# Optimization experiments

Hardware: AMD Instinct MI355X
Metric: run time of the kernel (lower is better)

Reference implementation:

```python
import jax, jax.numpy as jnp
import numpy as np

D_MODEL, HEADS, GROUPS, DIM_HEAD = 256, 8, 8, 64
INNER = HEADS * DIM_HEAD              # 512
OFF_DIMS = INNER // GROUPS            # 64 channels fed to the offset network per group
DF, OFF_SCALE, KS, PAD = 4, 4.0, 6, 1  # downsample_factor, offset_scale, kernel, (6-4)//2
CPB_DIM = D_MODEL // 4                # 64
NUM_LAYERS = 6
SCALE = DIM_HEAD ** -0.5
B, H, W = 1, 40, 40


def grouped_conv1x1(x, w, g):
    # x: (b, cin, h, w); w: (cout, cin//g) torch grouped 1x1 conv weight (squeezed)
    b, cin, h, wd = x.shape
    cout = w.shape[0]
    xg = x.reshape(b, g, cin // g, h, wd)
    wg = w.reshape(g, cout // g, cin // g)
    return jnp.einsum('goi,bgihw->bgohw', wg, xg).reshape(b, cout, h, wd)


def create_grid(h, w, dtype):
    # torch meshgrid(arange(w), arange(h), indexing='xy') stacked at dim 0
    ys, xs = jnp.meshgrid(jnp.arange(h, dtype=dtype), jnp.arange(w, dtype=dtype), indexing='ij')
    return jnp.stack((xs, ys))  # (2, h, w): channel0 = x, channel1 = y


def normalize_grid(grid):
    # faithful to source: channel0 scaled by (h-1), channel1 by (w-1); out dim last
    h, w = grid.shape[-2:]
    g0 = 2.0 * grid[..., 0, :, :] / max(h - 1, 1) - 1.0
    g1 = 2.0 * grid[..., 1, :, :] / max(w - 1, 1) - 1.0
    return jnp.stack((g0, g1), axis=-1)


def grid_sample_bilinear(img, grid):
    # torch F.grid_sample, mode='bilinear', padding_mode='zeros', align_corners=False
    Bn, C, Hh, Ww = img.shape
    gx = ((grid[..., 0] + 1.0) * Ww - 1.0) * 0.5
    gy = ((grid[..., 1] + 1.0) * Hh - 1.0) * 0.5
    x0 = jnp.floor(gx)
    y0 = jnp.floor(gy)
    wx1 = gx - x0
    wy1 = gy - y0
    flat = img.reshape(Bn, C, Hh * Ww)

    def gather(xi, yi):
        valid = (xi >= 0) & (xi <= Ww - 1) & (yi >= 0) & (yi <= Hh - 1)
        xc = jnp.clip(xi, 0, Ww - 1).astype(jnp.int32)
        yc = jnp.clip(yi, 0, Hh - 1).astype(jnp.int32)
        idx = (yc * Ww + xc).reshape(Bn, 1, -1)
        vals = jnp.take_along_axis(flat, idx, axis=2).reshape(Bn, C, *xi.shape[1:])
        return vals * valid[:, None].astype(img.dtype)

    return (gather(x0, y0) * ((1 - wx1) * (1 - wy1))[:, None]
            + gather(x0 + 1, y0) * (wx1 * (1 - wy1))[:, None]
            + gather(x0, y0 + 1) * ((1 - wx1) * wy1)[:, None]
            + gather(x0 + 1, y0 + 1) * (wx1 * wy1)[:, None])


def deform_attn(x, wq, wk, wv, w_off1, b_off1, w_off2,
                cpb_w0, cpb_b0, cpb_w1, cpb_b1, cpb_w2, cpb_b2, w_out, b_out):
    b, c, Hh, Ww = x.shape
    bg = b * GROUPS
    q = grouped_conv1x1(x, wq, GROUPS)                      # (b, 512, H, W)
    qg = q.reshape(bg, OFF_DIMS, Hh, Ww)                    # group heads: (b g) d h w
    # offset network: depthwise 6x6 stride-4 conv -> GELU -> 1x1 -> tanh * scale
    off = jax.lax.conv_general_dilated(
        qg, w_off1, (DF, DF), ((PAD, PAD), (PAD, PAD)),
        dimension_numbers=('NCHW', 'OIHW', 'NCHW'), feature_group_count=OFF_DIMS)
    off = jax.nn.gelu(off + b_off1[None, :, None, None], approximate=False)
    off = jnp.tanh(jnp.einsum('oc,bchw->bohw', w_off2, off)) * OFF_SCALE  # (bg,2,h',w')
    hp, wp = off.shape[-2:]
    vgrid = create_grid(hp, wp, x.dtype)[None] + off
    vgrid_scaled = normalize_grid(vgrid)                    # (bg, h', w', 2)
    xg = x.reshape(bg, c // GROUPS, Hh, Ww)
    kv = grid_sample_bilinear(xg, vgrid_scaled).reshape(b, c, hp, wp)
    k = grouped_conv1x1(kv, wk, GROUPS)
    v = grouped_conv1x1(kv, wv, GROUPS)
    i, j = Hh * Ww, hp * wp
    qh = (q * SCALE).reshape(b, HEADS, DIM_HEAD, i).transpose(0, 1, 3, 2)  # bhid
    kh = k.reshape(b, HEADS, DIM_HEAD, j).transpose(0, 1, 3, 2)
    vh = v.reshape(b, HEADS, DIM_HEAD, j).transpose(0, 1, 3, 2)
    sim = jnp.einsum('bhid,bhjd->bhij', qh, kh)
    # continuous positional bias (CPB, depth-2 MLP on signed-log relative coords)
    grid_q = normalize_grid(create_grid(Hh, Ww, x.dtype)).reshape(i, 2)
    grid_kv = vgrid_scaled.reshape(bg, j, 2)
    pos = grid_q[None, :, None, :] - grid_kv[:, None, :, :]  # (bg, i, j, 2)
    bias = jnp.sign(pos) * jnp.log1p(jnp.abs(pos))
    bias = jax.nn.relu(bias @ cpb_w0.T + cpb_b0)
    bias = jax.nn.relu(bias @ cpb_w1.T + cpb_b1)
    bias = bias @ cpb_w2.T + cpb_b2                          # (bg, i, j, 1)
    sim = sim + bias.reshape(b, GROUPS, i, j)                # heads//offset_groups == 1
    attn = jax.nn.softmax(sim, axis=-1)                      # stable softmax (matches amax-subtract)
    out = jnp.einsum('bhij,bhjd->bhid', attn, vh)
    out = out.transpose(0, 1, 3, 2).reshape(b, INNER, Hh, Ww)
    return jnp.einsum('oc,bchw->bohw', w_out, out) + b_out[None, :, None, None]


def setup_inputs() -> dict:
    key = jax.random.key(0)
    ks = jax.random.split(key, 16)
    L = NUM_LAYERS

    def p(k, shape, scale=0.02):
        return jax.random.normal(k, shape, dtype=jnp.float32) * scale

    return {
        'bev_feat': jax.random.normal(ks[0], (B, D_MODEL, H, W), dtype=jnp.float32),
        'wq': p(ks[1], (L, INNER, D_MODEL // GROUPS)),
        'wk': p(ks[2], (L, INNER, D_MODEL // GROUPS)),
        'wv': p(ks[3], (L, INNER, D_MODEL // GROUPS)),
        'w_off1': p(ks[4], (L, OFF_DIMS, 1, KS, KS)),
        'b_off1': jnp.zeros((L, OFF_DIMS), jnp.float32),
        'w_off2': p(ks[5], (L, 2, OFF_DIMS)),
        'cpb_w0': p(ks[6], (L, CPB_DIM, 2), 0.5),
        'cpb_b0': jnp.zeros((L, CPB_DIM), jnp.float32),
        'cpb_w1': p(ks[7], (L, CPB_DIM, CPB_DIM), 0.1),
        'cpb_b1': jnp.zeros((L, CPB_DIM), jnp.float32),
        'cpb_w2': p(ks[8], (L, 1, CPB_DIM), 0.1),
        'cpb_b2': jnp.zeros((L, 1), jnp.float32),
        'w_out': p(ks[9], (L, D_MODEL, INNER)),
        'b_out': jnp.zeros((L, D_MODEL), jnp.float32),
    }


def reference(bev_feat, wq, wk, wv, w_off1, b_off1, w_off2,
              cpb_w0, cpb_b0, cpb_w1, cpb_b1, cpb_w2, cpb_b2, w_out, b_out):
    # The source encoder loop runs `output = layer(bev_feat)` on the ORIGINAL
    # input each iteration, so only the last layer's output survives. Faithful
    # math = apply layer NUM_LAYERS-1 once (dropout in eval mode -> identity).
    l = NUM_LAYERS - 1
    return deform_attn(bev_feat, wq[l], wk[l], wv[l], w_off1[l], b_off1[l], w_off2[l],
                       cpb_w0[l], cpb_b0[l], cpb_w1[l], cpb_b1[l], cpb_w2[l], cpb_b2[l],
                       w_out[l], b_out[l])
```

## Files before the change

kernel.cpp:

```cpp
#include <hip/hip_runtime.h>
#include <math.h>


#define NP 1600
#define NJ 100

typedef _Float16 f16x8 __attribute__((ext_vector_type(8)));
typedef _Float16 f16x4 __attribute__((ext_vector_type(4)));
typedef _Float16 f16x2 __attribute__((ext_vector_type(2)));
typedef float  f32x4  __attribute__((ext_vector_type(4)));
typedef float  f32x2  __attribute__((ext_vector_type(2)));

template<int CTRL>
__device__ __forceinline__ float dpp_add(float x) {
  int y = __builtin_amdgcn_update_dpp(0, __builtin_bit_cast(int, x),
                                      CTRL, 0xf, 0xf, true);
  return x + __builtin_bit_cast(float, y);
}

__global__ __launch_bounds__(256, 4) void k_off_cpb(
    const float* __restrict__ x, const float* __restrict__ wq,
    const float* __restrict__ wdw,
    const float* __restrict__ bdw, const float* __restrict__ wo2,
    const float* __restrict__ wk, const float* __restrict__ wv,
    const float* __restrict__ w0, const float* __restrict__ b0,
    const float* __restrict__ w1, const float* __restrict__ b1v,
    const float* __restrict__ cw2, const float* __restrict__ b2,
    float* __restrict__ kout, float* __restrict__ vout_t,
    _Float16* __restrict__ bias16) {
  __shared__ float x_lds[36][32];
  __shared__ float psum[4][72];
  __shared__ float su_l[40];
  __shared__ float sv_l[40];
  __shared__ _Float16 a16[40][72];
  __shared__ _Float16 c16[40][72];
  int b = blockIdx.x;
  int g = b & 7;
  int j = b >> 3;
  int gj = g * 100 + j;
  int t = threadIdx.x;
  int lane = t & 63;
  int wv_id = t >> 6;
  int oy = j / 10, ox = j - (j / 10) * 10;
  int row = lane & 15;
  int kgrp = lane >> 4;

  for (int idx = t; idx < 1152; idx += 256) {
    int tap = idx >> 5, ci = idx & 31;
    int ky = tap / 6, kx = tap - (tap / 6) * 6;
    int iy = oy * 4 - 1 + ky;
    int ix = ox * 4 - 1 + kx;
    float v = 0.f;
    if (iy >= 0 && iy < 40 && ix >= 0 && ix < 40)
      v = x[(g * 32 + ci) * NP + iy * 40 + ix];
    x_lds[tap][ci] = v;
  }
  __syncthreads();

  {
    float wqreg[32];
    const float* wqr = wq + (size_t)(g * 64 + lane) * 32;
#pragma unroll
    for (int q4 = 0; q4 < 8; ++q4) {
      f32x4 a = *(const f32x4*)(wqr + q4 * 4);
#pragma unroll
      for (int e = 0; e < 4; ++e) wqreg[q4 * 4 + e] = a[e];
    }
    float acc = 0.f;
#pragma unroll
    for (int tu = 0; tu < 9; ++tu) {
      int tt = wv_id * 9 + tu;
      float qv = 0.f;
#pragma unroll
      for (int q4 = 0; q4 < 8; ++q4) {
        f32x4 xv = *(const f32x4*)&x_lds[tt][q4 * 4];
#pragma unroll
        for (int e = 0; e < 4; ++e)
          qv = fmaf(wqreg[q4 * 4 + e], xv[e], qv);
      }
      acc = fmaf(wdw[lane * 36 + tt], qv, acc);
    }
    psum[wv_id][lane] = acc;
  }
  __syncthreads();

  if (wv_id == 0) {
    float accd = psum[0][lane] + psum[1][lane] + psum[2][lane] + psum[3][lane]
               + bdw[lane];
    float od = 0.5f * accd * (1.0f + erff(accd * 0.70710678118654752440f));
    float px = wo2[lane] * od, py = wo2[64 + lane] * od;
#pragma unroll
    for (int m = 1; m < 64; m <<= 1) {
      px += __shfl_xor(px, m);
      py += __shfl_xor(py, m);
    }
    float ax = tanhf(px) * 4.f;
    float ay = tanhf(py) * 4.f;
    float vx = (float)ox + ax;
    float vy = (float)oy + ay;
    float g0 = 2.f * vx / 9.f - 1.f;
    float g1 = 2.f * vy / 9.f - 1.f;
    if (lane < 40) {
      float qc = (float)lane * (2.f / 39.f) - 1.f;
      float u = qc - g0;
      float vv2 = qc - g1;
      su_l[lane] = copysignf(log1pf(fabsf(u)), u);
      sv_l[lane] = copysignf(log1pf(fabsf(vv2)), vv2);
    }
    float gx = ((g0 + 1.f) * 40.f - 1.f) * 0.5f;
    float gy = ((g1 + 1.f) * 40.f - 1.f) * 0.5f;
    float x0f = floorf(gx), y0f = floorf(gy);
    float wx = gx - x0f, wy = gy - y0f;
    bool mx0 = (x0f >= 0.f) && (x0f <= 39.f);
    bool mx1 = (x0f + 1.f >= 0.f) && (x0f + 1.f <= 39.f);
    bool my0 = (y0f >= 0.f) && (y0f <= 39.f);
    bool my1 = (y0f + 1.f >= 0.f) && (y0f + 1.f <= 39.f);
    int ix0 = (int)fminf(fmaxf(x0f, 0.f), 39.f);
    int ix1 = (int)fminf(fmaxf(x0f + 1.f, 0.f), 39.f);
    int iy0 = (int)fminf(fmaxf(y0f, 0.f), 39.f);
    int iy1 = (int)fminf(fmaxf(y0f + 1.f, 0.f), 39.f);
    float w00 = (1.f - wx) * (1.f - wy) * ((mx0 && my0) ? 1.f : 0.f);
    float w10 = wx * (1.f - wy) * ((mx1 && my0) ? 1.f : 0.f);
    float w01 = (1.f - wx) * wy * ((mx0 && my1) ? 1.f : 0.f);
    float w11 = wx * wy * ((mx1 && my1) ? 1.f : 0.f);
    int b00 = iy0 * 40 + ix0, b10 = iy0 * 40 + ix1;
    int b01 = iy1 * 40 + ix0, b11 = iy1 * 40 + ix1;
    float kvc = 0.f;
    if (lane < 32) {
      const float* xc = x + (g * 32 + lane) * NP;
      kvc = w00 * xc[b00] + w10 * xc[b10] + w01 * xc[b01] + w11 * xc[b11];
    }
    const float* wkr = wk + (g * 64 + lane) * 32;
    const float* wvr = wv + (g * 64 + lane) * 32;
    float wkreg[32], wvreg[32];
#pragma unroll
    for (int q4 = 0; q4 < 8; ++q4) {
      f32x4 a = *(const f32x4*)(wkr + q4 * 4);
      f32x4 bq = *(const f32x4*)(wvr + q4 * 4);
#pragma unroll
      for (int e = 0; e < 4; ++e) { wkreg[q4 * 4 + e] = a[e]; wvreg[q4 * 4 + e] = bq[e]; }
    }
    float kacc = 0.f, vacc = 0.f;
#pragma unroll
    for (int c = 0; c < 32; ++c) {
      float kvb = __shfl(kvc, c);
      kacc = fmaf(wkreg[c], kvb, kacc);
      vacc = fmaf(wvreg[c], kvb, vacc);
    }
    kout[(g * 64 + lane) * 100 + j] = kacc;
    vout_t[(size_t)gj * 64 + lane] = vacc;
  }
  __syncthreads();

  for (int idx = t; idx < 2560; idx += 256) {
    int xi = idx >> 6, kk = idx & 63;
    a16[xi][kk] = (_Float16)fmaf(w0[2 * kk], su_l[xi], b0[kk]);
    c16[xi][kk] = (_Float16)(w0[2 * kk + 1] * sv_l[xi]);
  }

  f16x8 B[4][2];
#pragma unroll
  for (int ct = 0; ct < 4; ++ct)
#pragma unroll
    for (int s = 0; s < 2; ++s)
#pragma unroll
      for (int e = 0; e < 8; ++e)
        B[ct][s][e] = (_Float16)w1[(ct * 16 + row) * 64 + s * 32 + kgrp * 8 + e];
  float b1c[4], w2c[4];
#pragma unroll
  for (int ct = 0; ct < 4; ++ct) {
    b1c[ct] = b1v[ct * 16 + row];
    w2c[ct] = cw2[ct * 16 + row];
  }
  float bb = b2[0];
  _Float16* outp = bias16 + (size_t)gj * 1600;
  __syncthreads();

  int it0 = wv_id * 25;
  int iy = wv_id * 10;
  int ix = row;
  f16x8 zero8 = {};
  for (int it = it0; it < it0 + 25; ++it) {
    f32x4 acc[4];
#pragma unroll
    for (int ct = 0; ct < 4; ++ct) {
      acc[ct][0] = 0.f; acc[ct][1] = 0.f; acc[ct][2] = 0.f; acc[ct][3] = 0.f;
    }
#pragma unroll
    for (int s = 0; s < 2; ++s) {
      f16x8 av = *(const f16x8*)&a16[ix][s * 32 + kgrp * 8];
      f16x8 cv = *(const f16x8*)&c16[iy][s * 32 + kgrp * 8];
      f16x8 A = __builtin_elementwise_max(av + cv, zero8);
#pragma unroll
      for (int ct = 0; ct < 4; ++ct)
        acc[ct] = __builtin_amdgcn_mfma_f32_16x16x32_f16(A, B[ct][s], acc[ct], 0, 0, 0);
    }
    float part[4];
#pragma unroll
    for (int ri = 0; ri < 4; ++ri) {
      float s2 = 0.f;
#pragma unroll
      for (int ct = 0; ct < 4; ++ct) {
        float val = acc[ct][ri] + b1c[ct];
        s2 = fmaf(w2c[ct], fmaxf(val, 0.f), s2);
      }
      part[ri] = s2;
    }
#pragma unroll
    for (int ri = 0; ri < 4; ++ri) {
      part[ri] = dpp_add<0xB1>(part[ri]);
      part[ri] = dpp_add<0x4E>(part[ri]);
      part[ri] = dpp_add<0x141>(part[ri]);
      part[ri] = dpp_add<0x140>(part[ri]);
    }
    if (row == 0) {
      f16x4 o;
      o[0] = (_Float16)(part[0] + bb); o[1] = (_Float16)(part[1] + bb);
      o[2] = (_Float16)(part[2] + bb); o[3] = (_Float16)(part[3] + bb);
      *(f16x4*)(outp + it * 16 + kgrp * 4) = o;
    }
    ix += 16;
    if (ix >= 40) { ix -= 40; ++iy; }
  }
}

__global__ __launch_bounds__(256) void k_attn(
    const float* __restrict__ x, const float* __restrict__ wq,
    const float* __restrict__ k, const float* __restrict__ v_t,
    const _Float16* __restrict__ bias16, float* __restrict__ inner) {
  __shared__ float v_lds[100][68];
  __shared__ float s_lds[16][100];
  __shared__ float q_lds[64][20];
  __shared__ float x_tile[32][16];
  int h = blockIdx.x / 100;
  int i0 = (blockIdx.x - h * 100) * 16;
  int t = threadIdx.x;
  for (int idx = t; idx < 6400; idx += 256) {
    int j = idx >> 6, d = idx & 63;
    v_lds[j][d] = v_t[(size_t)h * 6400 + idx];
  }
  for (int idx = t; idx < 512; idx += 256) {
    int ci = idx >> 4, i = idx & 15;
    x_tile[ci][i] = x[(h * 32 + ci) * NP + i0 + i];
  }
  __syncthreads();
  {
    int d = t & 63;
    int i4 = t >> 6;
    f32x4 wr[8];
#pragma unroll
    for (int qq = 0; qq < 8; ++qq)
      wr[qq] = *(const f32x4*)(wq + (size_t)(h * 64 + d) * 32 + qq * 4);
#pragma unroll
    for (int ii = 0; ii < 4; ++ii) {
      int i = i4 * 4 + ii;
      float acc = 0.f;
#pragma unroll
      for (int ci = 0; ci < 32; ++ci)
        acc = fmaf(wr[ci >> 2][ci & 3], x_tile[ci][i], acc);
      q_lds[d][i] = acc;
    }
  }
  __syncthreads();
  if (t < 200) {
    int ib = (t / 25) * 2, jb = (t % 25) * 4;
    const float* kp = k + h * 64 * 100 + jb;
    float a[2][4];
#pragma unroll
    for (int ii = 0; ii < 2; ++ii)
#pragma unroll
      for (int jj = 0; jj < 4; ++jj) a[ii][jj] = 0.f;
#pragma unroll 8
    for (int d = 0; d < 64; ++d) {
      f32x2 qv = *(const f32x2*)&q_lds[d][ib];
      f32x4 kv4 = *(const f32x4*)(kp + d * 100);
#pragma unroll
      for (int ii = 0; ii < 2; ++ii)
#pragma unroll
        for (int jj = 0; jj < 4; ++jj)
          a[ii][jj] = fmaf(qv[ii], kv4[jj], a[ii][jj]);
    }
    const _Float16* bcol = bias16 + (size_t)h * 100 * 1600;
#pragma unroll
    for (int jj = 0; jj < 4; ++jj) {
      f16x2 bv = *(const f16x2*)(bcol + (size_t)(jb + jj) * 1600 + i0 + ib);
#pragma unroll
      for (int ii = 0; ii < 2; ++ii)
        s_lds[ib + ii][jb + jj] = fmaf(a[ii][jj], 0.125f, (float)bv[ii]);
    }
  }
  __syncthreads();
  {
    int i = t >> 4, sub = t & 15;
    float m = -1e30f;
    for (int j = sub; j < 100; j += 16) m = fmaxf(m, s_lds[i][j]);
#pragma unroll
    for (int off = 1; off < 16; off <<= 1) m = fmaxf(m, __shfl_xor(m, off));
    float sum = 0.f;
    for (int j = sub; j < 100; j += 16) {
      float e = expf(s_lds[i][j] - m);
      s_lds[i][j] = e;
      sum += e;
    }
#pragma unroll
    for (int off = 1; off < 16; off <<= 1) sum += __shfl_xor(sum, off);
    float inv = 1.f / sum;
    for (int j = sub; j < 100; j += 16) s_lds[i][j] *= inv;
  }
  __syncthreads();
  {
    int i = t & 15, db = (t >> 4) * 4;
    float acc[4];
#pragma unroll
    for (int dd = 0; dd < 4; ++dd) acc[dd] = 0.f;
    for (int jc = 0; jc < 25; ++jc) {
      f32x4 sv = *(const f32x4*)&s_lds[i][jc * 4];
#pragma unroll
      for (int jj = 0; jj < 4; ++jj) {
        f32x4 vv = *(const f32x4*)&v_lds[jc * 4 + jj][db];
#pragma unroll
        for (int dd = 0; dd < 4; ++dd)
          acc[dd] = fmaf(sv[jj], vv[dd], acc[dd]);
      }
    }
#pragma unroll
    for (int dd = 0; dd < 4; ++dd)
      inner[(h * 64 + db + dd) * NP + i0 + i] = acc[dd];
  }
}

__global__ __launch_bounds__(256) void k_proj(
    const float* __restrict__ inner, const float* __restrict__ w,
    const float* __restrict__ bo, float* __restrict__ out) {
  int oc = blockIdx.x & 31;
  int pt = blockIdx.x >> 5;
  int t = threadIdx.x;
  int quad = __builtin_amdgcn_readfirstlane(t >> 6);
  int o0 = oc * 8 + quad * 2;
  int p = pt * 64 + (t & 63);
  const float* w0r = w + (size_t)o0 * 512;
  float a0 = 0.f, a1 = 0.f;
#pragma unroll 8
  for (int c = 0; c < 512; ++c) {
    float xv = inner[c * NP + p];
    a0 = fmaf(w0r[c], xv, a0);
    a1 = fmaf(w0r[512 + c], xv, a1);
  }
  out[(o0 + 0) * NP + p] = a0 + bo[o0 + 0];
  out[(o0 + 1) * NP + p] = a1 + bo[o0 + 1];
}

extern "C" void kernel_launch(void* const* d_in, const int* in_sizes, int n_in,
                              void* d_out, int out_size, void* d_ws, size_t ws_size,
                              hipStream_t stream) {
  int L = in_sizes[1] / (512 * 32);
  int l = L - 1;
  const float* x      = (const float*)d_in[0];
  const float* wq     = (const float*)d_in[1]  + (size_t)l * 512 * 32;
  const float* wk     = (const float*)d_in[2]  + (size_t)l * 512 * 32;
  const float* wv     = (const float*)d_in[3]  + (size_t)l * 512 * 32;
  const float* w_off1 = (const float*)d_in[4]  + (size_t)l * 64 * 36;
  const float* b_off1 = (const float*)d_in[5]  + (size_t)l * 64;
  const float* w_off2 = (const float*)d_in[6]  + (size_t)l * 2 * 64;
  const float* cpb_w0 = (const float*)d_in[7]  + (size_t)l * 64 * 2;
  const float* cpb_b0 = (const float*)d_in[8]  + (size_t)l * 64;
  const float* cpb_w1 = (const float*)d_in[9]  + (size_t)l * 64 * 64;
  const float* cpb_b1 = (const float*)d_in[10] + (size_t)l * 64;
  const float* cpb_w2 = (const float*)d_in[11] + (size_t)l * 64;
  const float* cpb_b2 = (const float*)d_in[12] + (size_t)l * 1;
  const float* w_out  = (const float*)d_in[13] + (size_t)l * 256 * 512;
  const float* b_out  = (const float*)d_in[14] + (size_t)l * 256;
  float* out = (float*)d_out;

  float* ws = (float*)d_ws;
  float*    k_ws    = ws;
  float*    vt_ws   = ws + 51200;
  _Float16* bias16  = (_Float16*)(ws + 102400);
  float*    inner   = ws + 742400;

  k_off_cpb<<<800, 256, 0, stream>>>(x, wq, w_off1, b_off1, w_off2, wk, wv,
                                     cpb_w0, cpb_b0, cpb_w1, cpb_b1, cpb_w2,
                                     cpb_b2, k_ws, vt_ws, bias16);
  k_attn<<<800, 256, 0, stream>>>(x, wq, k_ws, vt_ws, bias16, inner);
  k_proj<<<800, 256, 0, stream>>>(inner, w_out, b_out, out);
}
```

Baseline: 92.00 us.

## Fuse CPB bias MLP into attention kernel, drop fp16 bias buffer

```diff
diff --git a/kernel.cpp b/kernel.cpp
--- a/kernel.cpp
+++ b/kernel.cpp
@@ -6,8 +6,6 @@
 #define NJ 100
 
 typedef _Float16 f16x8 __attribute__((ext_vector_type(8)));
-typedef _Float16 f16x4 __attribute__((ext_vector_type(4)));
-typedef _Float16 f16x2 __attribute__((ext_vector_type(2)));
 typedef float  f32x4  __attribute__((ext_vector_type(4)));
 typedef float  f32x2  __attribute__((ext_vector_type(2)));
 
@@ -18,22 +16,15 @@
   return x + __builtin_bit_cast(float, y);
 }
 
-__global__ __launch_bounds__(256, 4) void k_off_cpb(
+__global__ __launch_bounds__(256) void k_offnet(
     const float* __restrict__ x, const float* __restrict__ wq,
     const float* __restrict__ wdw,
     const float* __restrict__ bdw, const float* __restrict__ wo2,
     const float* __restrict__ wk, const float* __restrict__ wv,
-    const float* __restrict__ w0, const float* __restrict__ b0,
-    const float* __restrict__ w1, const float* __restrict__ b1v,
-    const float* __restrict__ cw2, const float* __restrict__ b2,
     float* __restrict__ kout, float* __restrict__ vout_t,
-    _Float16* __restrict__ bias16) {
+    float* __restrict__ gkv) {
   __shared__ float x_lds[36][32];
   __shared__ float psum[4][72];
-  __shared__ float su_l[40];
-  __shared__ float sv_l[40];
-  __shared__ _Float16 a16[40][72];
-  __shared__ _Float16 c16[40][72];
   int b = blockIdx.x;
   int g = b & 7;
   int j = b >> 3;
@@ -42,8 +33,6 @@
   int lane = t & 63;
   int wv_id = t >> 6;
   int oy = j / 10, ox = j - (j / 10) * 10;
-  int row = lane & 15;
-  int kgrp = lane >> 4;
 
   for (int idx = t; idx < 1152; idx += 256) {
     int tap = idx >> 5, ci = idx & 31;
@@ -100,12 +89,9 @@
     float vy = (float)oy + ay;
     float g0 = 2.f * vx / 9.f - 1.f;
     float g1 = 2.f * vy / 9.f - 1.f;
-    if (lane < 40) {
-      float qc = (float)lane * (2.f / 39.f) - 1.f;
-      float u = qc - g0;
-      float vv2 = qc - g1;
-      su_l[lane] = copysignf(log1pf(fabsf(u)), u);
-      sv_l[lane] = copysignf(log1pf(fabsf(vv2)), vv2);
+    if (lane == 0) {
+      f32x2 gv; gv[0] = g0; gv[1] = g1;
+      *(f32x2*)(gkv + (size_t)gj * 2) = gv;
     }
     float gx = ((g0 + 1.f) * 40.f - 1.f) * 0.5f;
     float gy = ((g1 + 1.f) * 40.f - 1.f) * 0.5f;
@@ -150,91 +136,31 @@
     kout[(g * 64 + lane) * 100 + j] = kacc;
     vout_t[(size_t)gj * 64 + lane] = vacc;
   }
-  __syncthreads();
-
-  for (int idx = t; idx < 2560; idx += 256) {
-    int xi = idx >> 6, kk = idx & 63;
-    a16[xi][kk] = (_Float16)fmaf(w0[2 * kk], su_l[xi], b0[kk]);
-    c16[xi][kk] = (_Float16)(w0[2 * kk + 1] * sv_l[xi]);
-  }
-
-  f16x8 B[4][2];
-#pragma unroll
-  for (int ct = 0; ct < 4; ++ct)
-#pragma unroll
-    for (int s = 0; s < 2; ++s)
-#pragma unroll
-      for (int e = 0; e < 8; ++e)
-        B[ct][s][e] = (_Float16)w1[(ct * 16 + row) * 64 + s * 32 + kgrp * 8 + e];
-  float b1c[4], w2c[4];
-#pragma unroll
-  for (int ct = 0; ct < 4; ++ct) {
-    b1c[ct] = b1v[ct * 16 + row];
-    w2c[ct] = cw2[ct * 16 + row];
-  }
-  float bb = b2[0];
-  _Float16* outp = bias16 + (size_t)gj * 1600;
-  __syncthreads();
-
-  int it0 = wv_id * 25;
-  int iy = wv_id * 10;
-  int ix = row;
-  f16x8 zero8 = {};
-  for (int it = it0; it < it0 + 25; ++it) {
-    f32x4 acc[4];
-#pragma unroll
-    for (int ct = 0; ct < 4; ++ct) {
-      acc[ct][0] = 0.f; acc[ct][1] = 0.f; acc[ct][2] = 0.f; acc[ct][3] = 0.f;
-    }
-#pragma unroll
-    for (int s = 0; s < 2; ++s) {
-      f16x8 av = *(const f16x8*)&a16[ix][s * 32 + kgrp * 8];
-      f16x8 cv = *(const f16x8*)&c16[iy][s * 32 + kgrp * 8];
-      f16x8 A = __builtin_elementwise_max(av + cv, zero8);
-#pragma unroll
-      for (int ct = 0; ct < 4; ++ct)
-        acc[ct] = __builtin_amdgcn_mfma_f32_16x16x32_f16(A, B[ct][s], acc[ct], 0, 0, 0);
-    }
-    float part[4];
-#pragma unroll
-    for (int ri = 0; ri < 4; ++ri) {
-      float s2 = 0.f;
-#pragma unroll
-      for (int ct = 0; ct < 4; ++ct) {
-        float val = acc[ct][ri] + b1c[ct];
-        s2 = fmaf(w2c[ct], fmaxf(val, 0.f), s2);
-      }
-      part[ri] = s2;
-    }
-#pragma unroll
-    for (int ri = 0; ri < 4; ++ri) {
-      part[ri] = dpp_add<0xB1>(part[ri]);
-      part[ri] = dpp_add<0x4E>(part[ri]);
-      part[ri] = dpp_add<0x141>(part[ri]);
-      part[ri] = dpp_add<0x140>(part[ri]);
-    }
-    if (row == 0) {
-      f16x4 o;
-      o[0] = (_Float16)(part[0] + bb); o[1] = (_Float16)(part[1] + bb);
-      o[2] = (_Float16)(part[2] + bb); o[3] = (_Float16)(part[3] + bb);
-      *(f16x4*)(outp + it * 16 + kgrp * 4) = o;
-    }
-    ix += 16;
-    if (ix >= 40) { ix -= 40; ++iy; }
-  }
 }
 
 __global__ __launch_bounds__(256) void k_attn(
     const float* __restrict__ x, const float* __restrict__ wq,
     const float* __restrict__ k, const float* __restrict__ v_t,
-    const _Float16* __restrict__ bias16, float* __restrict__ inner) {
+    const float* __restrict__ gkv,
+    const float* __restrict__ w0, const float* __restrict__ b0,
+    const float* __restrict__ w1, const float* __restrict__ b1v,
+    const float* __restrict__ cw2, const float* __restrict__ b2,
+    float* __restrict__ inner) {
   __shared__ float v_lds[100][68];
   __shared__ float s_lds[16][100];
   __shared__ float q_lds[64][20];
   __shared__ float x_tile[32][16];
+  __shared__ float su_blk[100][16];
+  __shared__ float sv_blk[100][2];
   int h = blockIdx.x / 100;
   int i0 = (blockIdx.x - h * 100) * 16;
   int t = threadIdx.x;
+  int lane = t & 63;
+  int wv_id = t >> 6;
+  int row = lane & 15;
+  int kgrp = lane >> 4;
+  int iyA = i0 / 40;
+
   for (int idx = t; idx < 6400; idx += 256) {
     int j = idx >> 6, d = idx & 63;
     v_lds[j][d] = v_t[(size_t)h * 6400 + idx];
@@ -243,7 +169,51 @@
     int ci = idx >> 4, i = idx & 15;
     x_tile[ci][i] = x[(h * 32 + ci) * NP + i0 + i];
   }
-  __syncthreads();
+  for (int idx = t; idx < 1600; idx += 256) {
+    int j = idx >> 4, r = idx & 15;
+    float g0 = gkv[(size_t)(h * 100 + j) * 2];
+    int i = i0 + r;
+    int iy = i / 40;
+    int ix = i - iy * 40;
+    float qx = (float)ix * (2.f / 39.f) - 1.f;
+    float u = qx - g0;
+    su_blk[j][r] = copysignf(log1pf(fabsf(u)), u);
+  }
+  if (t < 200) {
+    int j = t >> 1, s = t & 1;
+    float g1 = gkv[(size_t)(h * 100 + j) * 2 + 1];
+    int iy = s ? ((i0 + 15) / 40) : iyA;
+    float qy = (float)iy * (2.f / 39.f) - 1.f;
+    float v2 = qy - g1;
+    sv_blk[j][s] = copysignf(log1pf(fabsf(v2)), v2);
+  }
+  float w0x[2][8], w0y[2][8], b0v[2][8];
+#pragma unroll
+  for (int s = 0; s < 2; ++s)
+#pragma unroll
+    for (int e = 0; e < 8; ++e) {
+      int kk = s * 32 + kgrp * 8 + e;
+      w0x[s][e] = w0[2 * kk];
+      w0y[s][e] = w0[2 * kk + 1];
+      b0v[s][e] = b0[kk];
+    }
+  f16x8 B[4][2];
+#pragma unroll
+  for (int ct = 0; ct < 4; ++ct)
+#pragma unroll
+    for (int s = 0; s < 2; ++s)
+#pragma unroll
+      for (int e = 0; e < 8; ++e)
+        B[ct][s][e] = (_Float16)w1[(ct * 16 + row) * 64 + s * 32 + kgrp * 8 + e];
+  float b1c[4], w2c[4];
+#pragma unroll
+  for (int ct = 0; ct < 4; ++ct) {
+    b1c[ct] = b1v[ct * 16 + row];
+    w2c[ct] = cw2[ct * 16 + row];
+  }
+  float bb = b2[0];
+  __syncthreads();
+
   {
     int d = t & 63;
     int i4 = t >> 6;
@@ -261,7 +231,56 @@
       q_lds[d][i] = acc;
     }
   }
-  __syncthreads();
+  {
+    int i_lane = i0 + row;
+    int sel = (i_lane / 40 != iyA) ? 1 : 0;
+    for (int jt = wv_id * 25; jt < wv_id * 25 + 25; ++jt) {
+      float su = su_blk[jt][row];
+      float sv = sv_blk[jt][sel];
+      f32x4 acc[4];
+#pragma unroll
+      for (int ct = 0; ct < 4; ++ct) {
+        acc[ct][0] = 0.f; acc[ct][1] = 0.f; acc[ct][2] = 0.f; acc[ct][3] = 0.f;
+      }
+#pragma unroll
+      for (int s = 0; s < 2; ++s) {
+        f16x8 A;
+#pragma unroll
+        for (int e = 0; e < 8; ++e) {
+          float h0 = fmaf(w0x[s][e], su, fmaf(w0y[s][e], sv, b0v[s][e]));
+          A[e] = (_Float16)fmaxf(h0, 0.f);
+        }
+#pragma unroll
+        for (int ct = 0; ct < 4; ++ct)
+          acc[ct] = __builtin_amdgcn_mfma_f32_16x16x32_f16(A, B[ct][s], acc[ct], 0, 0, 0);
+      }
+      float part[4];
+#pragma unroll
+      for (int ri = 0; ri < 4; ++ri) {
+        float s2 = 0.f;
+#pragma unroll
+        for (int ct = 0; ct < 4; ++ct) {
+          float val = acc[ct][ri] + b1c[ct];
+          s2 = fmaf(w2c[ct], fmaxf(val, 0.f), s2);
+        }
+        part[ri] = s2;
+      }
+#pragma unroll
+      for (int ri = 0; ri < 4; ++ri) {
+        part[ri] = dpp_add<0xB1>(part[ri]);
+        part[ri] = dpp_add<0x4E>(part[ri]);
+        part[ri] = dpp_add<0x141>(part[ri]);
+        part[ri] = dpp_add<0x140>(part[ri]);
+      }
+      if (row == 0) {
+#pragma unroll
+        for (int ri = 0; ri < 4; ++ri)
+          s_lds[kgrp * 4 + ri][jt] = part[ri] + bb;
+      }
+    }
+  }
+  __syncthreads();
+
   if (t < 200) {
     int ib = (t / 25) * 2, jb = (t % 25) * 4;
     const float* kp = k + h * 64 * 100 + jb;
@@ -280,14 +299,11 @@
         for (int jj = 0; jj < 4; ++jj)
           a[ii][jj] = fmaf(qv[ii], kv4[jj], a[ii][jj]);
     }
-    const _Float16* bcol = bias16 + (size_t)h * 100 * 1600;
-#pragma unroll
-    for (int jj = 0; jj < 4; ++jj) {
-      f16x2 bv = *(const f16x2*)(bcol + (size_t)(jb + jj) * 1600 + i0 + ib);
+#pragma unroll
+    for (int jj = 0; jj < 4; ++jj)
 #pragma unroll
       for (int ii = 0; ii < 2; ++ii)
-        s_lds[ib + ii][jb + jj] = fmaf(a[ii][jj], 0.125f, (float)bv[ii]);
-    }
+        s_lds[ib + ii][jb + jj] = fmaf(a[ii][jj], 0.125f, s_lds[ib + ii][jb + jj]);
   }
   __syncthreads();
   {
@@ -373,14 +389,15 @@
   float* out = (float*)d_out;
 
   float* ws = (float*)d_ws;
-  float*    k_ws    = ws;
-  float*    vt_ws   = ws + 51200;
-  _Float16* bias16  = (_Float16*)(ws + 102400);
-  float*    inner   = ws + 742400;
-
-  k_off_cpb<<<800, 256, 0, stream>>>(x, wq, w_off1, b_off1, w_off2, wk, wv,
-                                     cpb_w0, cpb_b0, cpb_w1, cpb_b1, cpb_w2,
-                                     cpb_b2, k_ws, vt_ws, bias16);
-  k_attn<<<800, 256, 0, stream>>>(x, wq, k_ws, vt_ws, bias16, inner);
+  float* k_ws    = ws;
+  float* vt_ws   = ws + 51200;
+  float* gkv     = ws + 102400;
+  float* inner   = ws + 104000;
+
+  k_offnet<<<800, 256, 0, stream>>>(x, wq, w_off1, b_off1, w_off2, wk, wv,
+                                    k_ws, vt_ws, gkv);
+  k_attn<<<800, 256, 0, stream>>>(x, wq, k_ws, vt_ws, gkv,
+                                  cpb_w0, cpb_b0, cpb_w1, cpb_b1, cpb_w2,
+                                  cpb_b2, inner);
   k_proj<<<800, 256, 0, stream>>>(inner, w_out, b_out, out);
 }
```

Result: slower. 103.5 us (+12.5%).
